# Kernel tuning notes

Measured on AMD Instinct MI355X. Metric: run time of the kernel, lower is better.

## Reference

```python
import jax, jax.numpy as jnp
import numpy as np

B, S, D, H = 2, 2048, 1024, 16
DEPTH = D // H


def setup_inputs() -> dict:
    key = jax.random.key(0)
    ks = jax.random.split(key, 8)
    w_scale = 0.02
    # causal mask: 1.0 where attention is NOT allowed (added as mask * -1e9)
    causal = jnp.triu(jnp.ones((S, S), dtype=jnp.float32), k=1)[None, None]  # [1,1,S,S]
    return {
        "q": jax.random.normal(ks[0], (B, S, D), dtype=jnp.float32),
        "k": jax.random.normal(ks[1], (B, S, D), dtype=jnp.float32),
        "v": jax.random.normal(ks[2], (B, S, D), dtype=jnp.float32),
        "mask": causal,
        "Wq": jax.random.normal(ks[3], (D, D), dtype=jnp.float32) * w_scale,
        "bq": jnp.zeros((D,), dtype=jnp.float32),
        "Wk": jax.random.normal(ks[4], (D, D), dtype=jnp.float32) * w_scale,
        "bk": jnp.zeros((D,), dtype=jnp.float32),
        "Wv": jax.random.normal(ks[5], (D, D), dtype=jnp.float32) * w_scale,
        "bv": jnp.zeros((D,), dtype=jnp.float32),
        "Wo": jax.random.normal(ks[6], (D, D), dtype=jnp.float32) * w_scale,
        "bo": jnp.zeros((D,), dtype=jnp.float32),
    }


def _split_heads(x):
    # [B,S,D] -> [B,H,S,depth]
    return x.reshape(B, S, H, DEPTH).transpose(0, 2, 1, 3)


def reference(q, k, v, mask, Wq, bq, Wk, bk, Wv, bv, Wo, bo):
    qh = _split_heads(q @ Wq + bq)
    kh = _split_heads(k @ Wk + bk)
    vh = _split_heads(v @ Wv + bv)
    scale = 1.0 / jnp.sqrt(jnp.asarray(DEPTH, dtype=qh.dtype))
    logits = jnp.einsum('bhqd,bhkd->bhqk', qh, kh) * scale  # [B,H,S,S]
    logits = logits + mask * (-1e9)
    attn = jax.nn.softmax(logits, axis=-1)
    out = jnp.einsum('bhqk,bhkd->bhqd', attn, vh)  # [B,H,S,depth]
    out = out.transpose(0, 2, 1, 3).reshape(B, S, D)
    return out @ Wo + bo
```

## Files before the change

kernel.cpp:

```cpp
#include <hip/hip_runtime.h>


typedef unsigned short u16;
typedef unsigned int u32;

using bf16x8 = __attribute__((ext_vector_type(8))) short;
using bf16x4 = __attribute__((ext_vector_type(4))) short;
using f32x4  = __attribute__((ext_vector_type(4))) float;

#define SEQ 2048
#define DMODEL 1024
#define NHEAD 16
#define DEPTH 64
#define BATCH 2
#define M_ROWS (BATCH * SEQ)

__device__ __forceinline__ u16 f2bf(float f) {
    union { float f; u32 u; } v; v.f = f;
    u32 u = v.u;
    return (u16)((u + 0x7FFFu + ((u >> 16) & 1u)) >> 16);
}
__device__ __forceinline__ u16 f2bf_trunc(float f) {
    union { float f; u32 u; } v; v.f = f;
    return (u16)(v.u >> 16);
}

__device__ __forceinline__ float hw_exp2(float x) {
#if __has_builtin(__builtin_amdgcn_exp2f)
    return __builtin_amdgcn_exp2f(x);
#else
    float r;
    asm("v_exp_f32 %0, %1" : "=v"(r) : "v"(x));
    return r;
#endif
}

__device__ __forceinline__ f32x4 mfma16(bf16x8 a, bf16x8 b, f32x4 c) {
    return __builtin_amdgcn_mfma_f32_16x16x32_bf16(a, b, c, 0, 0, 0);
}

__device__ __forceinline__ void glds16(const u16* src, u16* dst) {
    __builtin_amdgcn_global_load_lds((const __attribute__((address_space(1))) void*)src,
                                     (__attribute__((address_space(3))) void*)dst,
                                     16, 0, 0);
}

__device__ __forceinline__ bf16x8 fragld(const u16* base, int lr, int gc) {
    return *(const bf16x8*)(base + lr * 64 + (((gc ^ lr) & 7) << 3));
}
__device__ __forceinline__ bf16x8 fragld32(const u16* base, int lr, int gc) {
    return *(const bf16x8*)(base + lr * 32 + (((gc ^ lr) & 3) << 3));
}

__global__ void cvt3_kernel(const float* __restrict__ q, const float* __restrict__ k,
                            const float* __restrict__ v,
                            u16* __restrict__ qo, u16* __restrict__ ko, u16* __restrict__ vo) {
    const float* in; u16* out;
    if (blockIdx.z == 0)      { in = q; out = qo; }
    else if (blockIdx.z == 1) { in = k; out = ko; }
    else                      { in = v; out = vo; }
    int idx = blockIdx.x * blockDim.x + threadIdx.x;
    float4 val = ((const float4*)in)[idx];
    ushort4 o;
    o.x = f2bf(val.x); o.y = f2bf(val.y); o.z = f2bf(val.z); o.w = f2bf(val.w);
    ((ushort4*)out)[idx] = o;
}

__global__ void wtrans_kernel(const float* __restrict__ Wq, const float* __restrict__ Wk,
                              const float* __restrict__ Wv, const float* __restrict__ Wo,
                              u16* __restrict__ Wqt, u16* __restrict__ Wkt,
                              u16* __restrict__ Wvt, u16* __restrict__ Wot) {
    __shared__ float tile[32][33];
    const float* W; u16* Wt;
    switch (blockIdx.z) {
        case 0: W = Wq; Wt = Wqt; break;
        case 1: W = Wk; Wt = Wkt; break;
        case 2: W = Wv; Wt = Wvt; break;
        default: W = Wo; Wt = Wot; break;
    }
    int k0 = blockIdx.x * 32, n0 = blockIdx.y * 32;
    int tx = threadIdx.x, ty = threadIdx.y;
#pragma unroll
    for (int i = 0; i < 4; ++i)
        tile[ty + 8 * i][tx] = W[(size_t)(k0 + ty + 8 * i) * DMODEL + n0 + tx];
    __syncthreads();
#pragma unroll
    for (int i = 0; i < 4; ++i)
        Wt[(size_t)(n0 + ty + 8 * i) * DMODEL + k0 + tx] = f2bf(tile[tx][ty + 8 * i]);
}

template<int TM>
__device__ __forceinline__ void gemm_core(const u16* __restrict__ A, const u16* __restrict__ Bt,
                                          const float* __restrict__ bias,
                                          u16* __restrict__ outb, float* __restrict__ outf,
                                          int mode, float oscale, int bm0, int bn0) {
    constexpr int K = DMODEL;
    constexpr int NT = K / 32;
    constexpr int MI = TM / 32;
    constexpr int ACH = TM / 64;
    __shared__ u16 As[2][TM * 32];
    __shared__ u16 Bs[2][128 * 32];
    int t = threadIdx.x;
    int w = t >> 6, lane = t & 63, l15 = lane & 15, quad = lane >> 4;
    int wm = (w >> 1) * (TM / 2), wn = (w & 1) * 64;
    int r16 = lane >> 2, g4 = lane & 3;
    int gswz = ((g4 ^ (r16 & 3)) << 3);
    f32x4 acc[MI][4] = {};

#define QSTAGE(p, kt) do { \
    _Pragma("unroll") for (int c = 0; c < ACH; ++c) { \
        int ch = w * ACH + c; \
        glds16(A + (size_t)(bm0 + ch * 16 + r16) * K + (kt) * 32 + gswz, &As[p][ch * 512]); } \
    _Pragma("unroll") for (int c = 0; c < 2; ++c) { \
        int ch = w * 2 + c; \
        glds16(Bt + (size_t)(bn0 + ch * 16 + r16) * K + (kt) * 32 + gswz, &Bs[p][ch * 512]); } \
    } while (0)

    QSTAGE(0, 0);
    __syncthreads();

    for (int kt = 0; kt < NT; ++kt) {
        int cur = kt & 1;
        if (kt + 1 < NT) QSTAGE(cur ^ 1, kt + 1);
        bf16x8 af[MI], bfr[4];
#pragma unroll
        for (int i = 0; i < MI; ++i) af[i]  = fragld32(&As[cur][0], wm + i * 16 + l15, quad);
#pragma unroll
        for (int j = 0; j < 4;  ++j) bfr[j] = fragld32(&Bs[cur][0], wn + j * 16 + l15, quad);
#pragma unroll
        for (int i = 0; i < MI; ++i)
#pragma unroll
            for (int j = 0; j < 4; ++j)
                acc[i][j] = mfma16(af[i], bfr[j], acc[i][j]);
        __syncthreads();
    }
#undef QSTAGE

#pragma unroll
    for (int i = 0; i < MI; ++i) {
        int row_g0 = bm0 + wm + i * 16 + quad * 4;
#pragma unroll
        for (int j = 0; j < 4; ++j) {
            int col_g = bn0 + wn + j * 16 + l15;
            float bsv = bias[col_g];
#pragma unroll
            for (int r = 0; r < 4; ++r) {
                float v = (acc[i][j][r] + bsv) * oscale;
                int rg = row_g0 + r;
                if (mode == 2) {
                    outf[(size_t)rg * DMODEL + col_g] = v;
                } else {
                    int b = rg >> 11, s = rg & (SEQ - 1);
                    int h = col_g >> 6, d = col_g & 63;
                    size_t idx;
                    if (mode == 0) idx = ((size_t)(b * NHEAD + h) * SEQ + s) * DEPTH + d;
                    else           idx = ((size_t)(b * NHEAD + h) * DEPTH + d) * SEQ + s;
                    outb[idx] = f2bf(v);
                }
            }
        }
    }
}

#define SCALE_Q 0.1803368801111204f

__global__ __launch_bounds__(256, 4) void gemm_qkv(
        const u16* __restrict__ qb, const u16* __restrict__ kb, const u16* __restrict__ vb,
        const u16* __restrict__ Wqt, const u16* __restrict__ Wkt, const u16* __restrict__ Wvt,
        const float* __restrict__ bq, const float* __restrict__ bk, const float* __restrict__ bv,
        u16* __restrict__ Qp, u16* __restrict__ Kp, u16* __restrict__ Vpt) {
    int id = blockIdx.x;
    int c = id & 7, m = id >> 3;
    int slab = c * 12 + (m >> 3);
    int x = m & 7;
    int z = slab >> 5, y = slab & 31;
    int bm0 = y * 128, bn0 = x * 128;
    if (z == 0)      gemm_core<128>(qb, Wqt, bq, Qp,  nullptr, 0, SCALE_Q, bm0, bn0);
    else if (z == 1) gemm_core<128>(kb, Wkt, bk, Kp,  nullptr, 0, 1.0f,    bm0, bn0);
    else             gemm_core<128>(vb, Wvt, bv, Vpt, nullptr, 1, 1.0f,    bm0, bn0);
}

__global__ __launch_bounds__(256, 4) void gemm_out(
        const u16* __restrict__ attnb, const u16* __restrict__ Wot,
        const float* __restrict__ bo, float* __restrict__ out) {
    int id = blockIdx.x;
    int c = id & 7, m = id >> 3;
    int slab = c * 8 + (m >> 3);
    int x = m & 7;
    gemm_core<64>(attnb, Wot, bo, nullptr, out, 2, 1.0f, slab * 64, x * 128);
}

#define LP 72
__global__ __launch_bounds__(256) void attn_kernel(
        const u16* __restrict__ Qp, const u16* __restrict__ Kp,
        const u16* __restrict__ Vpt, u16* __restrict__ attn_out) {
    __shared__ u16 Klds[2][64 * 64];
    __shared__ u16 Vtlds[2][64 * 64];
    __shared__ u16 Plds[4 * 16 * LP];
    int t = threadIdx.x, w = t >> 6, lane = t & 63, l15 = lane & 15, quad = lane >> 4;
    int r8 = lane >> 3, g8 = lane & 7;
    int gswz = ((g8 ^ r8) << 3);
    u16* Pw = Plds + w * 16 * LP;

    int id = blockIdx.x;
    int xcd = id & 7, li = id >> 3;
    int bh = xcd * 4 + (li & 3);
    int pi = li >> 2;
    int b = bh >> 4, h = bh & 15;
    const u16* Qbase = Qp  + (size_t)bh * SEQ * DEPTH;
    const u16* Kbase = Kp  + (size_t)bh * SEQ * DEPTH;
    const u16* Vbase = Vpt + (size_t)bh * DEPTH * SEQ;

    bf16x8 ones;
#pragma unroll
    for (int i = 0; i < 8; ++i) ones[i] = (short)0x3F80;

    for (int half = 0; half < 2; ++half) {
        int qt = half ? pi : (31 - pi);
        int q0 = qt * 64;
        int nkt = qt + 1;
        __syncthreads();

        int qrow = q0 + w * 16 + l15;
        bf16x8 qf[2];
        qf[0] = *(const bf16x8*)(Qbase + (size_t)qrow * DEPTH + quad * 8);
        qf[1] = *(const bf16x8*)(Qbase + (size_t)qrow * DEPTH + 32 + quad * 8);

        f32x4 of[4] = {};
        f32x4 lacc = {};

#pragma unroll
        for (int c2 = 0; c2 < 2; ++c2) {
            int ch = w * 2 + c2;
            glds16(Kbase + (size_t)(ch * 8 + r8) * DEPTH + gswz, Klds[0] + ch * 512);
            glds16(Vbase + (size_t)(ch * 8 + r8) * SEQ + gswz,   Vtlds[0] + ch * 512);
        }

        for (int kt = 0; kt < nkt; ++kt) {
            int cur = kt & 1;
            __syncthreads();
            if (kt + 1 < nkt) {
                int nx = cur ^ 1, kn = kt + 1;
#pragma unroll
                for (int c2 = 0; c2 < 2; ++c2) {
                    int ch = w * 2 + c2;
                    glds16(Kbase + (size_t)(kn * 64 + ch * 8 + r8) * DEPTH + gswz,
                           Klds[nx] + ch * 512);
                    glds16(Vbase + (size_t)(ch * 8 + r8) * SEQ + kn * 64 + gswz,
                           Vtlds[nx] + ch * 512);
                }
            }
            f32x4 st[4] = {};
            __builtin_amdgcn_s_setprio(1);
#pragma unroll
            for (int nt = 0; nt < 4; ++nt)
#pragma unroll
                for (int kk = 0; kk < 2; ++kk)
                    st[nt] = mfma16(fragld(Klds[cur], nt * 16 + l15, kk * 4 + quad), qf[kk], st[nt]);
            __builtin_amdgcn_s_setprio(0);

            bool diag = (kt == nkt - 1);
            int qlv = w * 16 + l15;
#pragma unroll
            for (int nt = 0; nt < 4; ++nt) {
                bf16x4 pv;
#pragma unroll
                for (int r = 0; r < 4; ++r) {
                    float e = hw_exp2(st[nt][r]);
                    if (diag) {
                        int keyl = nt * 16 + quad * 4 + r;
                        e = (keyl > qlv) ? 0.f : e;
                    }
                    pv[r] = (short)f2bf_trunc(e);
                }
                *(bf16x4*)(Pw + l15 * LP + nt * 16 + quad * 4) = pv;
            }
            asm volatile("" ::: "memory");
            bf16x8 pf[2];
            pf[0] = *(const bf16x8*)(Pw + l15 * LP + quad * 8);
            pf[1] = *(const bf16x8*)(Pw + l15 * LP + 32 + quad * 8);
            __builtin_amdgcn_s_setprio(1);
#pragma unroll
            for (int kk = 0; kk < 2; ++kk) {
                lacc = mfma16(pf[kk], ones, lacc);
#pragma unroll
                for (int nt = 0; nt < 4; ++nt)
                    of[nt] = mfma16(pf[kk], fragld(Vtlds[cur], nt * 16 + l15, kk * 4 + quad), of[nt]);
            }
            __builtin_amdgcn_s_setprio(0);
        }
#pragma unroll
        for (int r = 0; r < 4; ++r) {
            float inv = 1.0f / lacc[r];
            int s_ = q0 + w * 16 + quad * 4 + r;
#pragma unroll
            for (int nt = 0; nt < 4; ++nt) {
                int dcol = h * DEPTH + nt * 16 + l15;
                attn_out[((size_t)(b * SEQ + s_)) * DMODEL + dcol] = f2bf(of[nt][r] * inv);
            }
        }
    }
}

extern "C" void kernel_launch(void* const* d_in, const int* in_sizes, int n_in,
                              void* d_out, int out_size, void* d_ws, size_t ws_size,
                              hipStream_t stream) {
    const float* q  = (const float*)d_in[0];
    const float* k  = (const float*)d_in[1];
    const float* v  = (const float*)d_in[2];
    const float* Wq = (const float*)d_in[4];
    const float* bq = (const float*)d_in[5];
    const float* Wk = (const float*)d_in[6];
    const float* bk = (const float*)d_in[7];
    const float* Wv = (const float*)d_in[8];
    const float* bv = (const float*)d_in[9];
    const float* Wo = (const float*)d_in[10];
    const float* bo = (const float*)d_in[11];
    float* out = (float*)d_out;

    char* ws = (char*)d_ws;
    const size_t SZ_ACT = (size_t)M_ROWS * DMODEL * 2;
    const size_t SZ_W   = (size_t)DMODEL * DMODEL * 2;
    u16* qb   = (u16*)(ws);
    u16* kb   = (u16*)(ws + SZ_ACT);
    u16* vb   = (u16*)(ws + 2 * SZ_ACT);
    u16* Wqt  = (u16*)(ws + 3 * SZ_ACT);
    u16* Wkt  = (u16*)(ws + 3 * SZ_ACT + SZ_W);
    u16* Wvt  = (u16*)(ws + 3 * SZ_ACT + 2 * SZ_W);
    u16* Wot  = (u16*)(ws + 3 * SZ_ACT + 3 * SZ_W);
    u16* Qp   = (u16*)(ws + 3 * SZ_ACT + 4 * SZ_W);
    u16* Kp   = (u16*)(ws + 4 * SZ_ACT + 4 * SZ_W);
    u16* Vpt  = (u16*)(ws + 5 * SZ_ACT + 4 * SZ_W);
    u16* attnb= (u16*)(ws + 6 * SZ_ACT + 4 * SZ_W);

    cvt3_kernel<<<dim3(4096, 1, 3), 256, 0, stream>>>(q, k, v, qb, kb, vb);
    wtrans_kernel<<<dim3(32, 32, 4), dim3(32, 8), 0, stream>>>(Wq, Wk, Wv, Wo, Wqt, Wkt, Wvt, Wot);
    gemm_qkv<<<dim3(768), 256, 0, stream>>>(
        qb, kb, vb, Wqt, Wkt, Wvt, bq, bk, bv, Qp, Kp, Vpt);
    attn_kernel<<<dim3(512), 256, 0, stream>>>(Qp, Kp, Vpt, attnb);
    gemm_out<<<dim3(512), 256, 0, stream>>>(attnb, Wot, bo, out);
}
```

Measured before the change: 222.6 us.

## Software-pipeline PV MFMA behind next QK tile and merge prep kernels

The attention loop now defers the P·V and row-sum MFMAs of each key tile to the next iteration, issuing them after the current tile's QK MFMAs. This lets the exp/mask/P-store work overlap matrix work. V tiles use a triple-buffered LDS ring so the deferred tile stays valid while the next one is prefetched. The input conversion and weight transpose kernels are merged into one launch to remove a kernel boundary. The extra LDS buffer increases shared memory per block, which may lower occupancy.

```diff
diff --git a/kernel.cpp b/kernel.cpp
--- a/kernel.cpp
+++ b/kernel.cpp
@@ -52,41 +52,47 @@
     return *(const bf16x8*)(base + lr * 32 + (((gc ^ lr) & 3) << 3));
 }
 
-__global__ void cvt3_kernel(const float* __restrict__ q, const float* __restrict__ k,
-                            const float* __restrict__ v,
-                            u16* __restrict__ qo, u16* __restrict__ ko, u16* __restrict__ vo) {
-    const float* in; u16* out;
-    if (blockIdx.z == 0)      { in = q; out = qo; }
-    else if (blockIdx.z == 1) { in = k; out = ko; }
-    else                      { in = v; out = vo; }
-    int idx = blockIdx.x * blockDim.x + threadIdx.x;
-    float4 val = ((const float4*)in)[idx];
-    ushort4 o;
-    o.x = f2bf(val.x); o.y = f2bf(val.y); o.z = f2bf(val.z); o.w = f2bf(val.w);
-    ((ushort4*)out)[idx] = o;
-}
-
-__global__ void wtrans_kernel(const float* __restrict__ Wq, const float* __restrict__ Wk,
-                              const float* __restrict__ Wv, const float* __restrict__ Wo,
-                              u16* __restrict__ Wqt, u16* __restrict__ Wkt,
-                              u16* __restrict__ Wvt, u16* __restrict__ Wot) {
-    __shared__ float tile[32][33];
-    const float* W; u16* Wt;
-    switch (blockIdx.z) {
-        case 0: W = Wq; Wt = Wqt; break;
-        case 1: W = Wk; Wt = Wkt; break;
-        case 2: W = Wv; Wt = Wvt; break;
-        default: W = Wo; Wt = Wot; break;
+__global__ __launch_bounds__(256) void prep_kernel(
+        const float* __restrict__ q, const float* __restrict__ k,
+        const float* __restrict__ v,
+        u16* __restrict__ qo, u16* __restrict__ ko, u16* __restrict__ vo,
+        const float* __restrict__ Wq, const float* __restrict__ Wk,
+        const float* __restrict__ Wv, const float* __restrict__ Wo,
+        u16* __restrict__ Wqt, u16* __restrict__ Wkt,
+        u16* __restrict__ Wvt, u16* __restrict__ Wot) {
+    int bid = blockIdx.x;
+    if (bid < 12288) {
+        const float* in; u16* out;
+        int z = bid >> 12, bx = bid & 4095;
+        if (z == 0)      { in = q; out = qo; }
+        else if (z == 1) { in = k; out = ko; }
+        else             { in = v; out = vo; }
+        int idx = bx * 256 + threadIdx.x;
+        float4 val = ((const float4*)in)[idx];
+        ushort4 o;
+        o.x = f2bf(val.x); o.y = f2bf(val.y); o.z = f2bf(val.z); o.w = f2bf(val.w);
+        ((ushort4*)out)[idx] = o;
+    } else {
+        __shared__ float tile[32][33];
+        int wid = bid - 12288;
+        int z = wid >> 10, rem = wid & 1023;
+        const float* W; u16* Wt;
+        switch (z) {
+            case 0: W = Wq; Wt = Wqt; break;
+            case 1: W = Wk; Wt = Wkt; break;
+            case 2: W = Wv; Wt = Wvt; break;
+            default: W = Wo; Wt = Wot; break;
+        }
+        int k0 = (rem & 31) * 32, n0 = (rem >> 5) * 32;
+        int tx = threadIdx.x & 31, ty = threadIdx.x >> 5;
+#pragma unroll
+        for (int i = 0; i < 4; ++i)
+            tile[ty + 8 * i][tx] = W[(size_t)(k0 + ty + 8 * i) * DMODEL + n0 + tx];
+        __syncthreads();
+#pragma unroll
+        for (int i = 0; i < 4; ++i)
+            Wt[(size_t)(n0 + ty + 8 * i) * DMODEL + k0 + tx] = f2bf(tile[tx][ty + 8 * i]);
     }
-    int k0 = blockIdx.x * 32, n0 = blockIdx.y * 32;
-    int tx = threadIdx.x, ty = threadIdx.y;
-#pragma unroll
-    for (int i = 0; i < 4; ++i)
-        tile[ty + 8 * i][tx] = W[(size_t)(k0 + ty + 8 * i) * DMODEL + n0 + tx];
-    __syncthreads();
-#pragma unroll
-    for (int i = 0; i < 4; ++i)
-        Wt[(size_t)(n0 + ty + 8 * i) * DMODEL + k0 + tx] = f2bf(tile[tx][ty + 8 * i]);
 }
 
 template<int TM>
@@ -195,7 +201,7 @@
         const u16* __restrict__ Qp, const u16* __restrict__ Kp,
         const u16* __restrict__ Vpt, u16* __restrict__ attn_out) {
     __shared__ u16 Klds[2][64 * 64];
-    __shared__ u16 Vtlds[2][64 * 64];
+    __shared__ u16 Vtlds[3][64 * 64];
     __shared__ u16 Plds[4 * 16 * LP];
     int t = threadIdx.x, w = t >> 6, lane = t & 63, l15 = lane & 15, quad = lane >> 4;
     int r8 = lane >> 3, g8 = lane & 7;
@@ -228,6 +234,7 @@
 
         f32x4 of[4] = {};
         f32x4 lacc = {};
+        bf16x8 pfp[2];
 
 #pragma unroll
         for (int c2 = 0; c2 < 2; ++c2) {
@@ -237,17 +244,17 @@
         }
 
         for (int kt = 0; kt < nkt; ++kt) {
-            int cur = kt & 1;
+            int kc = kt & 1;
             __syncthreads();
             if (kt + 1 < nkt) {
-                int nx = cur ^ 1, kn = kt + 1;
+                int kn = kt + 1, knx = kn & 1, vnx = kn % 3;
 #pragma unroll
                 for (int c2 = 0; c2 < 2; ++c2) {
                     int ch = w * 2 + c2;
                     glds16(Kbase + (size_t)(kn * 64 + ch * 8 + r8) * DEPTH + gswz,
-                           Klds[nx] + ch * 512);
+                           Klds[knx] + ch * 512);
                     glds16(Vbase + (size_t)(ch * 8 + r8) * SEQ + kn * 64 + gswz,
-                           Vtlds[nx] + ch * 512);
+                           Vtlds[vnx] + ch * 512);
                 }
             }
             f32x4 st[4] = {};
@@ -256,8 +263,21 @@
             for (int nt = 0; nt < 4; ++nt)
 #pragma unroll
                 for (int kk = 0; kk < 2; ++kk)
-                    st[nt] = mfma16(fragld(Klds[cur], nt * 16 + l15, kk * 4 + quad), qf[kk], st[nt]);
+                    st[nt] = mfma16(fragld(Klds[kc], nt * 16 + l15, kk * 4 + quad), qf[kk], st[nt]);
             __builtin_amdgcn_s_setprio(0);
+
+            if (kt > 0) {
+                int vp = (kt - 1) % 3;
+                __builtin_amdgcn_s_setprio(1);
+#pragma unroll
+                for (int kk = 0; kk < 2; ++kk) {
+                    lacc = mfma16(pfp[kk], ones, lacc);
+#pragma unroll
+                    for (int nt = 0; nt < 4; ++nt)
+                        of[nt] = mfma16(pfp[kk], fragld(Vtlds[vp], nt * 16 + l15, kk * 4 + quad), of[nt]);
+                }
+                __builtin_amdgcn_s_setprio(0);
+            }
 
             bool diag = (kt == nkt - 1);
             int qlv = w * 16 + l15;
@@ -276,16 +296,18 @@
                 *(bf16x4*)(Pw + l15 * LP + nt * 16 + quad * 4) = pv;
             }
             asm volatile("" ::: "memory");
-            bf16x8 pf[2];
-            pf[0] = *(const bf16x8*)(Pw + l15 * LP + quad * 8);
-            pf[1] = *(const bf16x8*)(Pw + l15 * LP + 32 + quad * 8);
+            pfp[0] = *(const bf16x8*)(Pw + l15 * LP + quad * 8);
+            pfp[1] = *(const bf16x8*)(Pw + l15 * LP + 32 + quad * 8);
+        }
+        {
+            int vp = (nkt - 1) % 3;
             __builtin_amdgcn_s_setprio(1);
 #pragma unroll
             for (int kk = 0; kk < 2; ++kk) {
-                lacc = mfma16(pf[kk], ones, lacc);
+                lacc = mfma16(pfp[kk], ones, lacc);
 #pragma unroll
                 for (int nt = 0; nt < 4; ++nt)
-                    of[nt] = mfma16(pf[kk], fragld(Vtlds[cur], nt * 16 + l15, kk * 4 + quad), of[nt]);
+                    of[nt] = mfma16(pfp[kk], fragld(Vtlds[vp], nt * 16 + l15, kk * 4 + quad), of[nt]);
             }
             __builtin_amdgcn_s_setprio(0);
         }
@@ -333,8 +355,8 @@
     u16* Vpt  = (u16*)(ws + 5 * SZ_ACT + 4 * SZ_W);
     u16* attnb= (u16*)(ws + 6 * SZ_ACT + 4 * SZ_W);
 
-    cvt3_kernel<<<dim3(4096, 1, 3), 256, 0, stream>>>(q, k, v, qb, kb, vb);
-    wtrans_kernel<<<dim3(32, 32, 4), dim3(32, 8), 0, stream>>>(Wq, Wk, Wv, Wo, Wqt, Wkt, Wvt, Wot);
+    prep_kernel<<<dim3(16384), 256, 0, stream>>>(q, k, v, qb, kb, vb,
+                                                 Wq, Wk, Wv, Wo, Wqt, Wkt, Wvt, Wot);
     gemm_qkv<<<dim3(768), 256, 0, stream>>>(
         qb, kb, vb, Wqt, Wkt, Wvt, bq, bk, bv, Qp, Kp, Vpt);
     attn_kernel<<<dim3(512), 256, 0, stream>>>(Qp, Kp, Vpt, attnb);
```

Result: no change. 219.0 us (median of 3 runs) (-1.6%).
